# Performance work log

Measured on AMD Instinct MI355X. Metric: run time of the kernel, lower is better.

## Reference

```python
import jax, jax.numpy as jnp
import numpy as np

B, D, K = 16384, 512, 8192
COMMITMENT_COST = 0.25


def setup_inputs() -> dict:
    key = jax.random.key(0)
    k1, k2 = jax.random.split(key)
    z = jax.random.normal(k1, (B, D), dtype=jnp.float32)
    embedding = jax.random.normal(k2, (K, D), dtype=jnp.float32)
    return {"z": z, "embedding": embedding}


def reference(z, embedding):
    # Squared L2 distances: ||z||^2 - 2 z E^T + ||e||^2  -> [B, K]
    distances = (
        jnp.sum(z * z, axis=-1, keepdims=True)
        - 2.0 * jnp.matmul(z, embedding.T)
        + jnp.sum(embedding * embedding, axis=-1)
    )
    indices = jnp.argmin(distances, axis=-1)  # [B]
    quantized = embedding[indices]  # [B, D] gather
    # use_ema=True branch: commitment loss only (codebook updated by EMA)
    commitment_loss = jnp.mean((z - jax.lax.stop_gradient(quantized)) ** 2)
    loss = COMMITMENT_COST * commitment_loss
    # Straight-through estimator
    quantized_st = z + jax.lax.stop_gradient(quantized - z)
    return quantized_st, indices, loss
```

## Files before the change

### kernel.cpp

```cpp
#include <hip/hip_runtime.h>
#include <hip/hip_bf16.h>

#define M_ROWS 16384
#define N_CODES 8192
#define DDIM    512
#define NCHUNK  512
#define MARGIN  1.5f

typedef unsigned int u32;
typedef unsigned long long u64;
typedef unsigned short u16;
typedef __attribute__((ext_vector_type(8))) short short8;
typedef __attribute__((ext_vector_type(4))) float f32x4;

__device__ __forceinline__ u32 float_to_ordered(float f) {
    u32 u = __float_as_uint(f);
    return (u & 0x80000000u) ? ~u : (u | 0x80000000u);
}

__device__ __forceinline__ u16 bf16_rne(float x) {
    u32 u = __float_as_uint(x);
    u32 r = u + 0x7FFFu + ((u >> 16) & 1u);
    return (u16)(r >> 16);
}

__device__ __forceinline__ void gl_lds16(const void* g, void* l) {
    __builtin_amdgcn_global_load_lds((const __attribute__((address_space(1))) u32*)g,
                                     (__attribute__((address_space(3))) u32*)l,
                                     16, 0, 0);
}

__device__ __forceinline__ u64 umin64(u64 a, u64 b) { return a < b ? a : b; }

#if __has_builtin(__builtin_amdgcn_update_dpp)
template <int CTRL>
__device__ __forceinline__ float dpp_mov(float x) {
    return __int_as_float(__builtin_amdgcn_update_dpp(
        __float_as_int(x), __float_as_int(x), CTRL, 0xF, 0xF, true));
}
#else
template <int CTRL>
__device__ __forceinline__ float dpp_mov(float x) {
    return __shfl_xor(x, CTRL == 0xB1 ? 1 : 2, 64);
}
#endif

__global__ __launch_bounds__(256) void vq_prep(
    const float4* __restrict__ z4, ushort4* __restrict__ zh,
    const float* __restrict__ emb, ushort4* __restrict__ eh,
    float* __restrict__ e_norms) {
    int b = blockIdx.x;
    if (b < (M_ROWS * DDIM) / 1024) {
        int i = b * 256 + threadIdx.x;
        float4 v = z4[i];
        ushort4 h;
        h.x = bf16_rne(v.x); h.y = bf16_rne(v.y);
        h.z = bf16_rne(v.z); h.w = bf16_rne(v.w);
        zh[i] = h;
    } else {
        int wave = threadIdx.x >> 6;
        int lane = threadIdx.x & 63;
        int code = (b - (M_ROWS * DDIM) / 1024) * 4 + wave;
        const float4* ep = (const float4*)(emb + (size_t)code * DDIM);
        size_t base4 = (size_t)code * (DDIM / 4);
        float s = 0.f;
        #pragma unroll
        for (int j = 0; j < 2; ++j) {
            int c = lane + 64 * j;
            float4 e = ep[c];
            s += e.x * e.x + e.y * e.y + e.z * e.z + e.w * e.w;
            ushort4 h;
            h.x = bf16_rne(e.x); h.y = bf16_rne(e.y);
            h.z = bf16_rne(e.z); h.w = bf16_rne(e.w);
            eh[base4 + c] = h;
        }
        #pragma unroll
        for (int off = 32; off; off >>= 1) s += __shfl_down(s, off, 64);
        if (lane == 0) e_norms[code] = s;
    }
}

__device__ __forceinline__ void stage_tile(const char* gbase, int kt,
                                           void* lds, int tid) {
    #pragma unroll
    for (int s = 0; s < 4; ++s) {
        const int row_l = (s << 6) + (tid >> 3);
        const int cb = (((tid & 7) ^ (row_l & 7)) << 4);
        const char* g = gbase + (size_t)row_l * (DDIM * 2) + ((size_t)kt << 7) + cb;
        char* l = (char*)lds + (s << 13) + (tid << 4);
        gl_lds16(g, l);
    }
}

#define BAR() __builtin_amdgcn_s_barrier()
#define LGK0() do { asm volatile("s_waitcnt lgkmcnt(0)" ::: "memory"); \
                    __builtin_amdgcn_sched_barrier(0); } while (0)
#define VMC8() do { asm volatile("s_waitcnt vmcnt(8)" ::: "memory"); } while (0)
#define VMC0() do { asm volatile("s_waitcnt vmcnt(0)" ::: "memory"); } while (0)

#define LDA(BUF, MH) do {                                                      \
    _Pragma("unroll") for (int i_ = 0; i_ < 4; ++i_) {                         \
        _Pragma("unroll") for (int kk_ = 0; kk_ < 2; ++kk_) {                  \
            const int row_ = (wm << 7) + ((((MH) << 2) + i_) << 4) + fr;       \
            const int cb_ = (kk_ << 6) + fkb;                                  \
            a[i_][kk_] = *(const short8*)((const char*)&ldsA[BUF][0][0]        \
                + row_ * 128 + (cb_ ^ ((row_ & 7) << 4)));                     \
        } } } while (0)

#define LDB(BUF, NH) do {                                                      \
    _Pragma("unroll") for (int j_ = 0; j_ < 2; ++j_) {                         \
        _Pragma("unroll") for (int kk_ = 0; kk_ < 2; ++kk_) {                  \
            const int row_ = (wn << 6) + ((((NH) << 1) + j_) << 4) + fr;       \
            const int cb_ = (kk_ << 6) + fkb;                                  \
            b[(NH) * 2 + j_][kk_] = *(const short8*)((const char*)&ldsB[BUF][0][0] \
                + row_ * 128 + (cb_ ^ ((row_ & 7) << 4)));                     \
        } } } while (0)

#define MFMA_Q(MH, NH) do {                                                    \
    __builtin_amdgcn_s_setprio(1);                                             \
    _Pragma("unroll") for (int i_ = 0; i_ < 4; ++i_) {                         \
        _Pragma("unroll") for (int j_ = 0; j_ < 2; ++j_) {                     \
            _Pragma("unroll") for (int kk_ = 0; kk_ < 2; ++kk_) {              \
                acc[(MH) * 4 + i_][(NH) * 2 + j_] =                            \
                    __builtin_amdgcn_mfma_f32_16x16x32_bf16(                   \
                        a[i_][kk_], b[(NH) * 2 + j_][kk_],                     \
                        acc[(MH) * 4 + i_][(NH) * 2 + j_], 0, 0, 0);           \
        } } }                                                                  \
    __builtin_amdgcn_s_setprio(0);                                             \
} while (0)

#define PH_ITER(SE, VMA, VMB, NK0, NK1)                                        \
    LDA(0, 0); LDB(0, 0);                                                      \
    BAR(); LGK0(); MFMA_Q(0, 0); BAR();                                        \
    LDB(0, 1);                                                                 \
    BAR(); LGK0(); MFMA_Q(0, 1); BAR();                                        \
    LDA(0, 1);                                                                 \
    if (SE) stage_tile(gB0, (NK0), &ldsB[0][0][0], tid);                       \
    BAR(); LGK0(); MFMA_Q(1, 0); BAR();                                        \
    if (SE) stage_tile(gA0, (NK0), &ldsA[0][0][0], tid);                       \
    BAR(); MFMA_Q(1, 1); VMA; BAR();                                           \
    LDA(1, 0); LDB(1, 0);                                                      \
    BAR(); LGK0(); MFMA_Q(0, 0); BAR();                                        \
    LDB(1, 1);                                                                 \
    BAR(); LGK0(); MFMA_Q(0, 1); BAR();                                        \
    LDA(1, 1);                                                                 \
    if (SE) stage_tile(gB0, (NK1), &ldsB[1][0][0], tid);                       \
    BAR(); LGK0(); MFMA_Q(1, 0); BAR();                                        \
    if (SE) stage_tile(gA0, (NK1), &ldsA[1][0][0], tid);                       \
    BAR(); MFMA_Q(1, 1); VMB; BAR();

__global__ __launch_bounds__(512, 2) void vq_phase1(
    const u16* __restrict__ z_hi, const u16* __restrict__ e_hi,
    const float* __restrict__ e_norms,
    float* __restrict__ chunkmin) {
    __shared__ __align__(16) u16 ldsA[2][256][64];
    __shared__ __align__(16) u16 ldsB[2][256][64];

    const int tid  = threadIdx.x;
    const int lane = tid & 63;
    const int wid  = tid >> 6;
    const int wm   = wid >> 2;
    const int wn   = wid & 3;
    const int row0 = blockIdx.x << 8;
    const int col0 = blockIdx.y << 8;
    const int fr   = lane & 15;
    const int fkb  = (lane >> 4) << 4;

    const char* gA0 = (const char*)z_hi + (size_t)row0 * (DDIM * 2);
    const char* gB0 = (const char*)e_hi + (size_t)col0 * (DDIM * 2);

    f32x4 acc[8][4] = {};
    short8 a[4][2], b[4][2];

    stage_tile(gA0, 0, &ldsA[0][0][0], tid);
    stage_tile(gB0, 0, &ldsB[0][0][0], tid);
    stage_tile(gA0, 1, &ldsA[1][0][0], tid);
    stage_tile(gB0, 1, &ldsB[1][0][0], tid);
    VMC8(); BAR();

    #pragma unroll 1
    for (int t = 0; t < 3; ++t) {
        const int nk0 = 2 * t + 2, nk1 = 2 * t + 3;
        PH_ITER(1, VMC8(), VMC8(), nk0, nk1)
    }
    PH_ITER(0, VMC0(), ((void)0), 0, 0)

    const int cn = lane & 15;
    const int cg = lane >> 4;
    float en[4];
    #pragma unroll
    for (int j = 0; j < 4; ++j) en[j] = e_norms[col0 + (wn << 6) + j * 16 + cn];

    #pragma unroll
    for (int i = 0; i < 8; ++i)
        #pragma unroll
        for (int r = 0; r < 4; ++r) {
            float mv[4];
            #pragma unroll
            for (int j = 0; j < 4; ++j) mv[j] = en[j] - 2.0f * acc[i][j][r];

            #pragma unroll
            for (int k = 0; k < 2; ++k) {
                float lo = mv[k], hi = mv[k + 2];
                float mine = (lane & 8) ? hi : lo;
                float thrs = (lane & 8) ? lo : hi;
                mv[k] = fminf(mine, __shfl_xor(thrs, 8, 64));
            }
            {
                float lo = mv[0], hi = mv[1];
                float mine = (lane & 4) ? hi : lo;
                float thrs = (lane & 4) ? lo : hi;
                mv[0] = fminf(mine, __shfl_xor(thrs, 4, 64));
            }
            mv[0] = fminf(mv[0], dpp_mov<0xB1>(mv[0]));
            mv[0] = fminf(mv[0], dpp_mov<0x4E>(mv[0]));

            if ((cn & 3) == 0) {
                const int jj = ((cn >> 3) << 1) | ((cn >> 2) & 1);
                const int row_g = row0 + (wm << 7) + (i << 4) + (cg << 2) + r;
                chunkmin[(size_t)row_g * NCHUNK + (col0 >> 4) + (wn << 2) + jj] = mv[0];
            }
        }
}

__global__ __launch_bounds__(256) void vq_fin_a(
    float* __restrict__ chunkmin) {
    const int wave = threadIdx.x >> 6;
    const int lane = threadIdx.x & 63;
    const int row  = blockIdx.x * 4 + wave;

    float* cmrow = chunkmin + (size_t)row * NCHUNK;
    const float4* cm4 = (const float4*)cmrow;
    float4 v0 = cm4[lane];
    float4 v1 = cm4[64 + lane];
    float m = fminf(fminf(fminf(v0.x, v0.y), fminf(v0.z, v0.w)),
                    fminf(fminf(v1.x, v1.y), fminf(v1.z, v1.w)));
    #pragma unroll
    for (int off = 1; off < 64; off <<= 1) m = fminf(m, __shfl_xor(m, off, 64));
    const float thr = m + MARGIN;

    u64 msk[8];
    msk[0] = __ballot(v0.x <= thr);
    msk[1] = __ballot(v0.y <= thr);
    msk[2] = __ballot(v0.z <= thr);
    msk[3] = __ballot(v0.w <= thr);
    msk[4] = __ballot(v1.x <= thr);
    msk[5] = __ballot(v1.y <= thr);
    msk[6] = __ballot(v1.z <= thr);
    msk[7] = __ballot(v1.w <= thr);

    if (lane == 0) {
        u64* mrow = (u64*)cmrow;
        #pragma unroll
        for (int i = 0; i < 8; ++i) mrow[i] = msk[i];
    }
}

__global__ __launch_bounds__(256) void vq_fin_b(
    const float* __restrict__ z, const float* __restrict__ emb,
    const float* __restrict__ e_norms, const float* __restrict__ chunkmin,
    float* __restrict__ out_q, float* __restrict__ out_idx,
    float* __restrict__ partials) {
    const int wave = threadIdx.x >> 6;
    const int lane = threadIdx.x & 63;
    const int row  = blockIdx.x * 4 + wave;

    const u64* mrow = (const u64*)(chunkmin + (size_t)row * NCHUNK);
    u64 msk[8];
    #pragma unroll
    for (int i = 0; i < 8; ++i) msk[i] = mrow[i];

    const float4* z4 = (const float4*)(z + (size_t)row * DDIM);
    float4 za = z4[2 * lane];
    float4 zb = z4[2 * lane + 1];

    const int cown = ((lane & 1) << 3) | ((lane & 2) << 1)
                   | ((lane & 4) >> 1) | ((lane & 8) >> 3);

    u64 best = 0xFFFFFFFFFFFFFFFFull;
    #pragma unroll
    for (int p = 0; p < 2; ++p)
        #pragma unroll
        for (int j = 0; j < 4; ++j) {
            u64 mk = msk[p * 4 + j];
            while (mk) {
                int l = __ffsll((long long)mk) - 1;
                mk &= mk - 1;
                const int chunk = (p << 8) + (l << 2) + j;
                const int cbase = chunk << 4;
                const float* eb = emb + (size_t)cbase * DDIM + lane * 8;
                float part[16];
                #pragma unroll
                for (int k = 0; k < 16; ++k) {
                    float4 ea = *(const float4*)(eb + (size_t)k * DDIM);
                    float4 e2 = *(const float4*)(eb + (size_t)k * DDIM + 4);
                    part[k] = za.x * ea.x + za.y * ea.y + za.z * ea.z + za.w * ea.w
                            + zb.x * e2.x + zb.y * e2.y + zb.z * e2.z + zb.w * e2.w;
                }
                #pragma unroll
                for (int k = 0; k < 8; ++k) {
                    float lo = part[k], hi = part[k + 8];
                    float mine = (lane & 1) ? hi : lo;
                    float thrs = (lane & 1) ? lo : hi;
                    part[k] = mine + dpp_mov<0xB1>(thrs);
                }
                #pragma unroll
                for (int k = 0; k < 4; ++k) {
                    float lo = part[k], hi = part[k + 4];
                    float mine = (lane & 2) ? hi : lo;
                    float thrs = (lane & 2) ? lo : hi;
                    part[k] = mine + dpp_mov<0x4E>(thrs);
                }
                #pragma unroll
                for (int k = 0; k < 2; ++k) {
                    float lo = part[k], hi = part[k + 2];
                    float mine = (lane & 4) ? hi : lo;
                    float thrs = (lane & 4) ? lo : hi;
                    part[k] = mine + __shfl_xor(thrs, 4, 64);
                }
                {
                    float lo = part[0], hi = part[1];
                    float mine = (lane & 8) ? hi : lo;
                    float thrs = (lane & 8) ? lo : hi;
                    part[0] = mine + __shfl_xor(thrs, 8, 64);
                }
                part[0] += __shfl_xor(part[0], 16, 64);
                part[0] += __shfl_xor(part[0], 32, 64);

                const int ci = cbase + cown;
                float dist = e_norms[ci] - 2.0f * part[0];
                best = umin64(best, ((u64)float_to_ordered(dist) << 32) | (u32)ci);
            }
        }

    #pragma unroll
    for (int off = 1; off < 64; off <<= 1)
        best = umin64(best, __shfl_xor(best, off, 64));

    const int idx = (int)(best & 0xFFFFFFFFull);
    const float* ew = emb + (size_t)idx * DDIM + lane * 8;
    float4 qa = *(const float4*)ew;
    float4 qb = *(const float4*)(ew + 4);
    float4* op = (float4*)(out_q + (size_t)row * DDIM);
    op[2 * lane]     = qa;
    op[2 * lane + 1] = qb;

    float dx, local = 0.f;
    dx = za.x - qa.x; local += dx * dx;  dx = za.y - qa.y; local += dx * dx;
    dx = za.z - qa.z; local += dx * dx;  dx = za.w - qa.w; local += dx * dx;
    dx = zb.x - qb.x; local += dx * dx;  dx = zb.y - qb.y; local += dx * dx;
    dx = zb.z - qb.z; local += dx * dx;  dx = zb.w - qb.w; local += dx * dx;
    #pragma unroll
    for (int off = 32; off; off >>= 1) local += __shfl_down(local, off, 64);

    __shared__ float wsum[4];
    if (lane == 0) { wsum[wave] = local; out_idx[row] = (float)idx; }
    __syncthreads();
    if (threadIdx.x == 0)
        partials[blockIdx.x] = wsum[0] + wsum[1] + wsum[2] + wsum[3];
}

__global__ __launch_bounds__(256) void vq_loss_reduce(
    const float* __restrict__ partials, float* __restrict__ out_loss) {
    __shared__ float red[256];
    float s = 0.f;
    for (int i = threadIdx.x; i < M_ROWS / 4; i += 256) s += partials[i];
    red[threadIdx.x] = s;
    __syncthreads();
    for (int off = 128; off; off >>= 1) {
        if (threadIdx.x < off) red[threadIdx.x] += red[threadIdx.x + off];
        __syncthreads();
    }
    if (threadIdx.x == 0)
        out_loss[0] = 0.25f * red[0] / ((float)M_ROWS * (float)DDIM);
}

extern "C" void kernel_launch(void* const* d_in, const int* in_sizes, int n_in,
                              void* d_out, int out_size, void* d_ws, size_t ws_size,
                              hipStream_t stream) {
    (void)in_sizes; (void)n_in; (void)out_size; (void)ws_size;
    const float* z   = (const float*)d_in[0];
    const float* emb = (const float*)d_in[1];

    float* out      = (float*)d_out;
    float* out_q    = out;
    float* out_idx  = out + (size_t)M_ROWS * DDIM;
    float* out_loss = out + (size_t)M_ROWS * DDIM + M_ROWS;

    char* ws = (char*)d_ws;
    float* e_norms  = (float*)ws;
    float* partials = (float*)(ws + 32768);
    u16* z_hi = (u16*)(ws + 49152);
    u16* e_hi = (u16*)(ws + 49152 + (size_t)M_ROWS * DDIM * 2);

    float* chunkmin = out_q;

    const int zblocks = (M_ROWS * DDIM) / 1024;
    const int eblocks = N_CODES / 4;
    vq_prep<<<zblocks + eblocks, 256, 0, stream>>>(
        (const float4*)z, (ushort4*)z_hi, emb, (ushort4*)e_hi, e_norms);

    vq_phase1<<<dim3(M_ROWS / 256, N_CODES / 256), 512, 0, stream>>>(
        z_hi, e_hi, e_norms, chunkmin);

    vq_fin_a<<<M_ROWS / 4, 256, 0, stream>>>(chunkmin);

    vq_fin_b<<<M_ROWS / 4, 256, 0, stream>>>(
        z, emb, e_norms, chunkmin, out_q, out_idx, partials);

    vq_loss_reduce<<<1, 256, 0, stream>>>(partials, out_loss);
}
```

Before: 333.5 us.

## Refine candidate chunks to 8 codes with fp16-packed chunk minima

The GEMM epilogue now reduces distances over 8-code groups instead of 16 and packs two group minima as fp16 into each 32-bit chunkmin slot, keeping the intermediate buffer the same size. The finalize kernels unpack 16 values per lane, build 16 ballot masks, and rescore only the flagged 8-code groups in fp32. The intent is to cut the exact rescoring work by making candidate groups finer. In exchange, fp16 rounding of the minima forces a wider margin (2.5 instead of 1.5), which can admit more candidates, and fp16 could lose range for large distances.

```diff
diff --git a/kernel.cpp b/kernel.cpp
--- a/kernel.cpp
+++ b/kernel.cpp
@@ -1,11 +1,12 @@
 #include <hip/hip_runtime.h>
 #include <hip/hip_bf16.h>
+#include <hip/hip_fp16.h>
 
 #define M_ROWS 16384
 #define N_CODES 8192
 #define DDIM    512
 #define NCHUNK  512
-#define MARGIN  1.5f
+#define MARGIN  2.5f
 
 typedef unsigned int u32;
 typedef unsigned long long u64;
@@ -31,6 +32,13 @@
 }
 
 __device__ __forceinline__ u64 umin64(u64 a, u64 b) { return a < b ? a : b; }
+
+__device__ __forceinline__ float f16lo(u32 w) {
+    return __half2float(__ushort_as_half((unsigned short)(w & 0xFFFFu)));
+}
+__device__ __forceinline__ float f16hi(u32 w) {
+    return __half2float(__ushort_as_half((unsigned short)(w >> 16)));
+}
 
 #if __has_builtin(__builtin_amdgcn_update_dpp)
 template <int CTRL>
@@ -202,23 +210,26 @@
             #pragma unroll
             for (int k = 0; k < 2; ++k) {
                 float lo = mv[k], hi = mv[k + 2];
-                float mine = (lane & 8) ? hi : lo;
-                float thrs = (lane & 8) ? lo : hi;
-                mv[k] = fminf(mine, __shfl_xor(thrs, 8, 64));
+                float mine = (lane & 4) ? hi : lo;
+                float thrs = (lane & 4) ? lo : hi;
+                mv[k] = fminf(mine, __shfl_xor(thrs, 4, 64));
             }
             {
                 float lo = mv[0], hi = mv[1];
-                float mine = (lane & 4) ? hi : lo;
-                float thrs = (lane & 4) ? lo : hi;
-                mv[0] = fminf(mine, __shfl_xor(thrs, 4, 64));
+                float mine = (lane & 2) ? hi : lo;
+                float thrs = (lane & 2) ? lo : hi;
+                mv[0] = fminf(mine, __shfl_xor(thrs, 2, 64));
             }
             mv[0] = fminf(mv[0], dpp_mov<0xB1>(mv[0]));
-            mv[0] = fminf(mv[0], dpp_mov<0x4E>(mv[0]));
-
-            if ((cn & 3) == 0) {
-                const int jj = ((cn >> 3) << 1) | ((cn >> 2) & 1);
+            float other = __shfl_xor(mv[0], 8, 64);
+
+            if ((cn & 9) == 0) {
+                const int jj = (((cn >> 2) & 1) << 1) | ((cn >> 1) & 1);
+                u32 plo = (u32)__half_as_ushort(__float2half(mv[0]));
+                u32 phi = (u32)__half_as_ushort(__float2half(other));
                 const int row_g = row0 + (wm << 7) + (i << 4) + (cg << 2) + r;
-                chunkmin[(size_t)row_g * NCHUNK + (col0 >> 4) + (wn << 2) + jj] = mv[0];
+                chunkmin[(size_t)row_g * NCHUNK + (col0 >> 4) + (wn << 2) + jj] =
+                    __uint_as_float(plo | (phi << 16));
             }
         }
 }
@@ -233,26 +244,32 @@
     const float4* cm4 = (const float4*)cmrow;
     float4 v0 = cm4[lane];
     float4 v1 = cm4[64 + lane];
-    float m = fminf(fminf(fminf(v0.x, v0.y), fminf(v0.z, v0.w)),
-                    fminf(fminf(v1.x, v1.y), fminf(v1.z, v1.w)));
+
+    u32 w[8];
+    w[0] = __float_as_uint(v0.x); w[1] = __float_as_uint(v0.y);
+    w[2] = __float_as_uint(v0.z); w[3] = __float_as_uint(v0.w);
+    w[4] = __float_as_uint(v1.x); w[5] = __float_as_uint(v1.y);
+    w[6] = __float_as_uint(v1.z); w[7] = __float_as_uint(v1.w);
+
+    float vals[16];
+    #pragma unroll
+    for (int i = 0; i < 8; ++i) { vals[2 * i] = f16lo(w[i]); vals[2 * i + 1] = f16hi(w[i]); }
+
+    float m = vals[0];
+    #pragma unroll
+    for (int i = 1; i < 16; ++i) m = fminf(m, vals[i]);
     #pragma unroll
     for (int off = 1; off < 64; off <<= 1) m = fminf(m, __shfl_xor(m, off, 64));
     const float thr = m + MARGIN;
 
-    u64 msk[8];
-    msk[0] = __ballot(v0.x <= thr);
-    msk[1] = __ballot(v0.y <= thr);
-    msk[2] = __ballot(v0.z <= thr);
-    msk[3] = __ballot(v0.w <= thr);
-    msk[4] = __ballot(v1.x <= thr);
-    msk[5] = __ballot(v1.y <= thr);
-    msk[6] = __ballot(v1.z <= thr);
-    msk[7] = __ballot(v1.w <= thr);
+    u64 msk[16];
+    #pragma unroll
+    for (int k = 0; k < 16; ++k) msk[k] = __ballot(vals[k] <= thr);
 
     if (lane == 0) {
         u64* mrow = (u64*)cmrow;
         #pragma unroll
-        for (int i = 0; i < 8; ++i) mrow[i] = msk[i];
+        for (int i = 0; i < 16; ++i) mrow[i] = msk[i];
     }
 }
 
@@ -266,72 +283,66 @@
     const int row  = blockIdx.x * 4 + wave;
 
     const u64* mrow = (const u64*)(chunkmin + (size_t)row * NCHUNK);
-    u64 msk[8];
-    #pragma unroll
-    for (int i = 0; i < 8; ++i) msk[i] = mrow[i];
+    u64 msk[16];
+    #pragma unroll
+    for (int i = 0; i < 16; ++i) msk[i] = mrow[i];
 
     const float4* z4 = (const float4*)(z + (size_t)row * DDIM);
     float4 za = z4[2 * lane];
     float4 zb = z4[2 * lane + 1];
 
-    const int cown = ((lane & 1) << 3) | ((lane & 2) << 1)
-                   | ((lane & 4) >> 1) | ((lane & 8) >> 3);
+    const int cown = ((lane & 1) << 2) | (lane & 2) | ((lane >> 2) & 1);
 
     u64 best = 0xFFFFFFFFFFFFFFFFull;
     #pragma unroll
-    for (int p = 0; p < 2; ++p)
-        #pragma unroll
-        for (int j = 0; j < 4; ++j) {
-            u64 mk = msk[p * 4 + j];
-            while (mk) {
-                int l = __ffsll((long long)mk) - 1;
-                mk &= mk - 1;
-                const int chunk = (p << 8) + (l << 2) + j;
-                const int cbase = chunk << 4;
-                const float* eb = emb + (size_t)cbase * DDIM + lane * 8;
-                float part[16];
-                #pragma unroll
-                for (int k = 0; k < 16; ++k) {
-                    float4 ea = *(const float4*)(eb + (size_t)k * DDIM);
-                    float4 e2 = *(const float4*)(eb + (size_t)k * DDIM + 4);
-                    part[k] = za.x * ea.x + za.y * ea.y + za.z * ea.z + za.w * ea.w
-                            + zb.x * e2.x + zb.y * e2.y + zb.z * e2.z + zb.w * e2.w;
-                }
-                #pragma unroll
-                for (int k = 0; k < 8; ++k) {
-                    float lo = part[k], hi = part[k + 8];
-                    float mine = (lane & 1) ? hi : lo;
-                    float thrs = (lane & 1) ? lo : hi;
-                    part[k] = mine + dpp_mov<0xB1>(thrs);
-                }
-                #pragma unroll
-                for (int k = 0; k < 4; ++k) {
-                    float lo = part[k], hi = part[k + 4];
-                    float mine = (lane & 2) ? hi : lo;
-                    float thrs = (lane & 2) ? lo : hi;
-                    part[k] = mine + dpp_mov<0x4E>(thrs);
-                }
-                #pragma unroll
-                for (int k = 0; k < 2; ++k) {
-                    float lo = part[k], hi = part[k + 2];
-                    float mine = (lane & 4) ? hi : lo;
-                    float thrs = (lane & 4) ? lo : hi;
-                    part[k] = mine + __shfl_xor(thrs, 4, 64);
-                }
-                {
-                    float lo = part[0], hi = part[1];
-                    float mine = (lane & 8) ? hi : lo;
-                    float thrs = (lane & 8) ? lo : hi;
-                    part[0] = mine + __shfl_xor(thrs, 8, 64);
-                }
-                part[0] += __shfl_xor(part[0], 16, 64);
-                part[0] += __shfl_xor(part[0], 32, 64);
-
-                const int ci = cbase + cown;
-                float dist = e_norms[ci] - 2.0f * part[0];
-                best = umin64(best, ((u64)float_to_ordered(dist) << 32) | (u32)ci);
-            }
+    for (int wnd = 0; wnd < 16; ++wnd) {
+        const int p = wnd >> 3;
+        const int c = (wnd >> 1) & 3;
+        const int h = wnd & 1;
+        u64 mk = msk[wnd];
+        while (mk) {
+            int l = __ffsll((long long)mk) - 1;
+            mk &= mk - 1;
+            const int slot  = (p << 8) + (l << 2) + c;
+            const int cbase = ((slot << 1) + h) << 3;
+            const float* eb = emb + (size_t)cbase * DDIM + lane * 8;
+            float part[8];
+            #pragma unroll
+            for (int k = 0; k < 8; ++k) {
+                float4 ea = *(const float4*)(eb + (size_t)k * DDIM);
+                float4 e2 = *(const float4*)(eb + (size_t)k * DDIM + 4);
+                part[k] = za.x * ea.x + za.y * ea.y + za.z * ea.z + za.w * ea.w
+                        + zb.x * e2.x + zb.y * e2.y + zb.z * e2.z + zb.w * e2.w;
+            }
+            #pragma unroll
+            for (int k = 0; k < 4; ++k) {
+                float lo = part[k], hi = part[k + 4];
+                float mine = (lane & 1) ? hi : lo;
+                float thrs = (lane & 1) ? lo : hi;
+                part[k] = mine + dpp_mov<0xB1>(thrs);
+            }
+            #pragma unroll
+            for (int k = 0; k < 2; ++k) {
+                float lo = part[k], hi = part[k + 2];
+                float mine = (lane & 2) ? hi : lo;
+                float thrs = (lane & 2) ? lo : hi;
+                part[k] = mine + dpp_mov<0x4E>(thrs);
+            }
+            {
+                float lo = part[0], hi = part[1];
+                float mine = (lane & 4) ? hi : lo;
+                float thrs = (lane & 4) ? lo : hi;
+                part[0] = mine + __shfl_xor(thrs, 4, 64);
+            }
+            part[0] += __shfl_xor(part[0], 8, 64);
+            part[0] += __shfl_xor(part[0], 16, 64);
+            part[0] += __shfl_xor(part[0], 32, 64);
+
+            const int ci = cbase + cown;
+            float dist = e_norms[ci] - 2.0f * part[0];
+            best = umin64(best, ((u64)float_to_ordered(dist) << 32) | (u32)ci);
         }
+    }
 
     #pragma unroll
     for (int off = 1; off < 64; off <<= 1)
```

New measurement: 302.9 us. 9.2% less time.
